# Kernel optimization log

Measured on AMD Instinct MI355X. Metric: run time of the kernel, lower is better.

## Reference

```python
import jax, jax.numpy as jnp
import numpy as np

DIM = 1024; HEADS = 8; DHEAD = 64; INNER = HEADS * DHEAD
WS = 512; B = 2; N = 2048; FF = 4 * DIM
NEG = -1e9


def layernorm(x, g, b, eps=1e-5):
    mu = jnp.mean(x, -1, keepdims=True)
    var = jnp.mean((x - mu) ** 2, -1, keepdims=True)
    return (x - mu) * jax.lax.rsqrt(var + eps) * g + b


def rmsnorm(x, g, eps=1e-6):
    return x * jax.lax.rsqrt(jnp.mean(x * x, -1, keepdims=True) + eps) * g


def rotate_half(x):
    x1, x2 = jnp.split(x, 2, -1)
    return jnp.concatenate([-x2, x1], -1)


def local_attention(q, k, v):
    # lucidrains LocalAttention: single-head over last dim, rotary pos emb,
    # window_size=WS, causal, look_backward=1, look_forward=0. n % WS == 0 so autopad no-op.
    b, n, d = q.shape
    w = n // WS
    inv_freq = 1.0 / (10000.0 ** (jnp.arange(0, d, 2, dtype=jnp.float32) / d))
    t = jnp.arange(n)
    freqs = t[:, None].astype(jnp.float32) * inv_freq[None, :]
    emb = jnp.concatenate([freqs, freqs], -1)           # [n, d]
    cos, sin = jnp.cos(emb), jnp.sin(emb)
    q = q * cos + rotate_half(q) * sin
    k = k * cos + rotate_half(k) * sin
    bq = q.reshape(b, w, WS, d) * (d ** -0.5)
    bk = k.reshape(b, w, WS, d)
    bv = v.reshape(b, w, WS, d)

    def look_around(x, pad_value):
        # gather current window + 1 window backward along the window axis
        pads = [(0, 0), (1, 0)] + [(0, 0)] * (x.ndim - 2)
        xp = jnp.pad(x, pads, constant_values=pad_value)
        return jnp.concatenate([xp[:, 0:w], xp[:, 1:w + 1]], axis=2)

    bk = look_around(bk, 0.0)                 # [b, w, 2*WS, d]
    bv = look_around(bv, 0.0)
    bt = t.reshape(w, WS)                     # query positions per window
    bqk = look_around(bt[None], -1)[0]        # key positions, pad = -1  [w, 2*WS]
    sim = jnp.einsum('bwie,bwje->bwij', bq, bk)  # [b, w, WS, 2*WS]
    mask = (bt[:, :, None] < bqk[:, None, :]) | (bqk[:, None, :] == -1)
    sim = jnp.where(mask[None], NEG, sim)
    attn = jax.nn.softmax(sim, -1)
    out = jnp.einsum('bwij,bwje->bwie', attn, bv)
    return out.reshape(b, n, d)


def setup_inputs() -> dict:
    key = jax.random.key(0)
    ks = jax.random.split(key, 10)
    s = 0.02
    f32 = jnp.float32
    return {
        'text': jax.random.normal(ks[0], (B, N, DIM), f32),
        'audio': jax.random.normal(ks[1], (B, N, DIM), f32),
        'video': jax.random.normal(ks[2], (B, N, DIM), f32),
        'Wa': jax.random.normal(ks[3], (DIM, DIM), f32) * s,
        'ba': jnp.zeros((DIM,), f32),
        'lna_g': jnp.ones((DIM,), f32), 'lna_b': jnp.zeros((DIM,), f32),
        'Wvid': jax.random.normal(ks[4], (DIM, DIM), f32) * s,
        'bvid': jnp.zeros((DIM,), f32),
        'lnv_g': jnp.ones((DIM,), f32), 'lnv_b': jnp.zeros((DIM,), f32),
        'ln1_g': jnp.ones((DIM,), f32), 'ln1_b': jnp.zeros((DIM,), f32),
        'Wq': jax.random.normal(ks[5], (DIM, INNER), f32) * s,
        'Wkv': jax.random.normal(ks[6], (DIM, 2 * INNER), f32) * s,
        'qn_g': jnp.ones((DHEAD,), f32), 'kn_g': jnp.ones((DHEAD,), f32),
        'Wo': jax.random.normal(ks[7], (INNER, DIM), f32) * s,
        'W1': jax.random.normal(ks[8], (DIM, FF), f32) * s,
        'b1': jnp.zeros((FF,), f32),
        'ln2_g': jnp.ones((FF,), f32), 'ln2_b': jnp.zeros((FF,), f32),
        'W2': jax.random.normal(ks[9], (FF, DIM), f32) * s,
        'b2': jnp.zeros((DIM,), f32),
    }


def reference(text, audio, video, Wa, ba, lna_g, lna_b, Wvid, bvid, lnv_g, lnv_b,
              ln1_g, ln1_b, Wq, Wkv, qn_g, kn_g, Wo, W1, b1, ln2_g, ln2_b, W2, b2):
    # modality -> text-token adapters (audio_to_text / video_to_text): linear + layernorm
    audio_t = layernorm(audio @ Wa + ba, lna_g, lna_b)
    video_t = layernorm(video @ Wvid + bvid, lnv_g, lnv_b)
    # windowed local attention: q=text, k=audio tokens, v=video tokens
    x = local_attention(text, audio_t, video_t)          # [B, N, DIM]
    # qk-norm full causal attention (flash=False: dense [B,H,N,N] scores)
    b, n, _ = x.shape
    h = layernorm(x, ln1_g, ln1_b)
    q = (h @ Wq).reshape(b, n, HEADS, DHEAD).transpose(0, 2, 1, 3)
    k, v = jnp.split(h @ Wkv, 2, -1)
    k = k.reshape(b, n, HEADS, DHEAD).transpose(0, 2, 1, 3)
    v = v.reshape(b, n, HEADS, DHEAD).transpose(0, 2, 1, 3)
    q = rmsnorm(q, qn_g)
    k = rmsnorm(k, kn_g)
    sim = jnp.einsum('bhid,bhjd->bhij', q, k) * (DHEAD ** -0.5)
    causal = jnp.tril(jnp.ones((n, n), bool))
    sim = jnp.where(causal[None, None], sim, NEG)
    attn = jax.nn.softmax(sim, -1)
    o = jnp.einsum('bhij,bhjd->bhid', attn, v).transpose(0, 2, 1, 3).reshape(b, n, INNER)
    x = o @ Wo
    x = x + x                                            # x = x + x in source
    # FFN: Linear -> GELU -> post-act LayerNorm -> Linear, + residual
    h1 = layernorm(jax.nn.gelu(x @ W1 + b1), ln2_g, ln2_b)
    return h1 @ W2 + b2 + x
```

## Files before the change

### kernel.cpp

```cpp
#include <hip/hip_runtime.h>
#include <hip/hip_bf16.h>

typedef __bf16 bf16;
typedef __bf16 bf16x8 __attribute__((ext_vector_type(8)));
typedef float  f32x4  __attribute__((ext_vector_type(4)));

static __device__ __forceinline__ float b2f(bf16 x) { return (float)x; }
static __device__ __forceinline__ bf16  f2b(float x) { return (bf16)x; }
static __device__ __forceinline__ float ldval(float v) { return v; }
static __device__ __forceinline__ float ldval(bf16 v)  { return (float)v; }

static __device__ __forceinline__ void gl_lds16(const bf16* g, bf16* l)
{
    __builtin_amdgcn_global_load_lds(
        (const __attribute__((address_space(1))) void*)g,
        (__attribute__((address_space(3))) void*)l,
        16, 0, 0);
}

__global__ void detect_dtype(const unsigned short* __restrict__ p, int* __restrict__ flag)
{
    if (threadIdx.x == 0 && blockIdx.x == 0) {
        int big = 0;
        for (int i = 0; i < 512; ++i) {
            int e = (p[i] >> 7) & 0xFF;
            if (e >= 0xE0) big++;
        }
        *flag = (big > 0) ? 1 : 0;
    }
}

__global__ __launch_bounds__(256) void convert2(
    const void* __restrict__ sa, const void* __restrict__ sb,
    bf16* __restrict__ da, bf16* __restrict__ db, int n,
    const int* __restrict__ flag)
{
    int f = *flag;
    int half = gridDim.x >> 1;
    const void* s = (blockIdx.x < half) ? sa : sb;
    bf16* d = (blockIdx.x < half) ? da : db;
    int bid = (blockIdx.x < half) ? blockIdx.x : blockIdx.x - half;
    for (int i = bid * 256 + threadIdx.x; i < n; i += half * 256) {
        float v = f ? ((const float*)s)[i] : (float)((const bf16*)s)[i];
        d[i] = f2b(v);
    }
}

struct VecPack { const void* src[14]; int n[14]; };
__global__ __launch_bounds__(256) void convert_vecs(
    VecPack vp, bf16* __restrict__ dst, const int* __restrict__ flag)
{
    int v = blockIdx.x;
    int f = *flag;
    const void* s = vp.src[v];
    int n = vp.n[v];
    bf16* d = dst + (size_t)v * 4096;
    for (int i = threadIdx.x; i < n; i += 256) {
        float x = f ? ((const float*)s)[i] : (float)((const bf16*)s)[i];
        d[i] = f2b(x);
    }
}

template <int EPI, int MT>
__global__ __launch_bounds__(256) void gemm_bt(
    const bf16* __restrict__ A0, int lda, int zsA, int zsA2,
    const bf16* __restrict__ B0, int ldb, int zsB, int zsB2,
    void* __restrict__ C0, int ldc, int zsC, int zsC2,
    const bf16* __restrict__ bias, int zsBias, float scale, int K)
{
    constexpr int IFR = MT / 32;
    __shared__ __align__(16) bf16 As[MT * 64];
    __shared__ __align__(16) bf16 Bs[128 * 64];
    const int z = blockIdx.z;
    const bf16* A  = A0 + (size_t)z * zsA + (size_t)(z >> 2) * zsA2;
    const bf16* Bt = B0 + (size_t)z * zsB + (size_t)(z >> 2) * zsB2;
    const size_t cbase = (size_t)z * zsC + (size_t)(z >> 2) * zsC2;
    if (bias) bias += (size_t)z * zsBias;
    const int tid  = threadIdx.x;
    const int lane = tid & 63, wave = tid >> 6;
    const int quad = lane >> 4, l16 = lane & 15;
    const size_t tm = (size_t)blockIdx.y * MT, tn = (size_t)blockIdx.x * 128;
    const int wm = (wave >> 1) * (MT / 2), wn = (wave & 1) * 64;
    const int srow = lane >> 3;
    const int scol = ((lane & 7) ^ srow) * 8;

    f32x4 acc[IFR][4];
    const f32x4 zro = {0.f, 0.f, 0.f, 0.f};
    #pragma unroll
    for (int i = 0; i < IFR; ++i)
        #pragma unroll
        for (int j = 0; j < 4; ++j) acc[i][j] = zro;

    const int swzA = l16 & 7;
    for (int k0 = 0; k0 < K; k0 += 64) {
        #pragma unroll
        for (int i = 0; i < IFR; ++i) {
            int chunk = (wave * IFR + i) * 64;
            int row = (chunk >> 3) + srow;
            gl_lds16(A + (tm + row) * (size_t)lda + k0 + scol, As + (size_t)chunk * 8);
        }
        #pragma unroll
        for (int i = 0; i < 4; ++i) {
            int chunk = (wave * 4 + i) * 64;
            int row = (chunk >> 3) + srow;
            gl_lds16(Bt + (tn + row) * (size_t)ldb + k0 + scol, Bs + (size_t)chunk * 8);
        }
        __syncthreads();
        #pragma unroll
        for (int kk = 0; kk < 2; ++kk) {
            bf16x8 af[IFR], bfr[4];
            #pragma unroll
            for (int i = 0; i < IFR; ++i) {
                int row = wm + i * 16 + l16;
                af[i] = *(const bf16x8*)(const void*)&As[(row * 8 + ((kk*4 + quad) ^ swzA)) * 8];
            }
            #pragma unroll
            for (int j = 0; j < 4; ++j) {
                int row = wn + j * 16 + l16;
                bfr[j] = *(const bf16x8*)(const void*)&Bs[(row * 8 + ((kk*4 + quad) ^ swzA)) * 8];
            }
            #pragma unroll
            for (int i = 0; i < IFR; ++i)
                #pragma unroll
                for (int j = 0; j < 4; ++j)
                    acc[i][j] = __builtin_amdgcn_mfma_f32_16x16x32_bf16(
                        af[i], bfr[j], acc[i][j], 0, 0, 0);
        }
        __syncthreads();
    }

    float* Cf = (float*)C0;
    bf16*  Cb = (bf16*)C0;
    #pragma unroll
    for (int i = 0; i < IFR; ++i) {
        #pragma unroll
        for (int j = 0; j < 4; ++j) {
            size_t col = tn + wn + j*16 + l16;
            float bb = bias ? b2f(bias[col]) : 0.f;
            #pragma unroll
            for (int r = 0; r < 4; ++r) {
                size_t row = tm + wm + i*16 + quad*4 + r;
                float v = acc[i][j][r] + bb;
                size_t off = cbase + row * (size_t)ldc + col;
                if (EPI == 0) {
                    Cf[off] = v;
                } else if (EPI == 1) {
                    Cb[off] = f2b(v * scale);
                } else {
                    float g = 0.5f * v * (1.f + tanhf(0.7978845608028654f *
                                  (v + 0.044715f * v * v * v)));
                    Cb[off] = f2b(g);
                }
            }
        }
    }
}

__global__ __launch_bounds__(512, 2) void gemm_ff1_8ph(
    const bf16* __restrict__ A, int lda,
    const bf16* __restrict__ Bt, int ldb,
    bf16* __restrict__ C, int ldc,
    const bf16* __restrict__ bias, int K)
{
    __shared__ __align__(16) bf16 As[2][256 * 64];
    __shared__ __align__(16) bf16 Bs[2][256 * 64];
    const int tid  = threadIdx.x;
    const int lane = tid & 63, wave = tid >> 6;
    const int quad = lane >> 4, l16 = lane & 15;
    const int wr = wave >> 2, wc = wave & 3;
    const size_t tm = (size_t)blockIdx.y * 256;
    const size_t tn = (size_t)blockIdx.x * 256;
    const int srow = lane >> 3;
    const int scol = ((lane & 7) ^ srow) * 8;
    const int swz  = l16 & 7;

    f32x4 acc[8][4];
    const f32x4 zro = {0.f, 0.f, 0.f, 0.f};
    #pragma unroll
    for (int m = 0; m < 8; ++m)
        #pragma unroll
        for (int n = 0; n < 4; ++n) acc[m][n] = zro;

    const bf16* aSrc[4];
    const bf16* bSrc[4];
    #pragma unroll
    for (int i = 0; i < 4; ++i) {
        int grow = wave * 32 + i * 8 + srow;
        aSrc[i] = A  + (tm + grow) * (size_t)lda + scol;
        bSrc[i] = Bt + (tn + grow) * (size_t)ldb + scol;
    }

#define STAGE(BUF, K0, I)                                                     \
    do {                                                                      \
        gl_lds16(aSrc[I] + (K0), &As[BUF][(wave * 4 + (I)) * 512]);           \
        gl_lds16(bSrc[I] + (K0), &Bs[BUF][(wave * 4 + (I)) * 512]);           \
    } while (0)

#define LDA_F(BUF, M, KK)                                                     \
    (*(const bf16x8*)(const void*)&As[BUF][(wr * 128 + (M) * 16 + l16) * 64 + \
        ((((KK) * 4 + quad) ^ swz) << 3)])
#define LDB_F(BUF, N, KK)                                                     \
    (*(const bf16x8*)(const void*)&Bs[BUF][(wc * 64 + (N) * 16 + l16) * 64 +  \
        ((((KK) * 4 + quad) ^ swz) << 3)])

#define PHASE(M0, M1, PREF_STMT, TAIL_STMT)                                   \
    {                                                                         \
        PREF_STMT;                                                            \
        bf16x8 x0 = LDA_F(cur, M0, 0), x1 = LDA_F(cur, M0, 1);                \
        bf16x8 y0 = LDA_F(cur, M1, 0), y1 = LDA_F(cur, M1, 1);                \
        asm volatile("s_barrier" ::: "memory");                               \
        __builtin_amdgcn_s_setprio(1);                                        \
        _Pragma("unroll")                                                     \
        for (int n = 0; n < 4; ++n) {                                         \
            acc[M0][n] = __builtin_amdgcn_mfma_f32_16x16x32_bf16(x0, bfr[n][0], acc[M0][n], 0, 0, 0); \
            acc[M0][n] = __builtin_amdgcn_mfma_f32_16x16x32_bf16(x1, bfr[n][1], acc[M0][n], 0, 0, 0); \
            acc[M1][n] = __builtin_amdgcn_mfma_f32_16x16x32_bf16(y0, bfr[n][0], acc[M1][n], 0, 0, 0); \
            acc[M1][n] = __builtin_amdgcn_mfma_f32_16x16x32_bf16(y1, bfr[n][1], acc[M1][n], 0, 0, 0); \
        }                                                                     \
        __builtin_amdgcn_s_setprio(0);                                        \
        TAIL_STMT;                                                            \
        asm volatile("s_barrier" ::: "memory");                               \
    }

    #pragma unroll
    for (int i = 0; i < 4; ++i) STAGE(0, 0, i);
    asm volatile("s_waitcnt vmcnt(0)" ::: "memory");
    asm volatile("s_barrier" ::: "memory");

    const int NT = K >> 6;
    bf16x8 bfr[4][2];
    for (int t = 0; t < NT; ++t) {
        const int cur = t & 1, nxt = cur ^ 1;
        const int k1  = (t + 1) << 6;
        const bool pref = (t + 1 < NT);

        #pragma unroll
        for (int n = 0; n < 4; ++n) {
            bfr[n][0] = LDB_F(cur, n, 0);
            bfr[n][1] = LDB_F(cur, n, 1);
        }
        PHASE(0, 1,
              if (pref) { STAGE(nxt, k1, 0); STAGE(nxt, k1, 1); }, )
        PHASE(2, 3,
              if (pref) { STAGE(nxt, k1, 2); STAGE(nxt, k1, 3); }, )
        PHASE(4, 5, , )
        PHASE(6, 7, ,
              asm volatile("s_waitcnt vmcnt(0)" ::: "memory"))
    }
#undef PHASE
#undef LDB_F
#undef LDA_F
#undef STAGE

    #pragma unroll
    for (int m = 0; m < 8; ++m) {
        #pragma unroll
        for (int n = 0; n < 4; ++n) {
            size_t col = tn + wc * 64 + n * 16 + l16;
            float bb = b2f(bias[col]);
            #pragma unroll
            for (int r = 0; r < 4; ++r) {
                size_t row = tm + wr * 128 + m * 16 + quad * 4 + r;
                float v = acc[m][n][r] + bb;
                float s = v * (1.5957691216057308f + 0.07135481627f * v * v);
                float g = v / (1.f + __expf(-s));
                C[row * (size_t)ldc + col] = f2b(g);
            }
        }
    }
}

__global__ void transpose_any(const void* __restrict__ in, int R, int C,
                              unsigned short* __restrict__ out, int ldo,
                              const int* __restrict__ flag)
{
    __shared__ unsigned short t[32][33];
    int f = *flag;
    int c0 = blockIdx.x * 32, r0 = blockIdx.y * 32;
    int tx = threadIdx.x, ty = threadIdx.y;
    for (int i = ty; i < 32; i += 8) {
        size_t idx = (size_t)(r0 + i) * C + c0 + tx;
        bf16 v = f ? f2b(((const float*)in)[idx]) : ((const bf16*)in)[idx];
        t[i][tx] = *(unsigned short*)&v;
    }
    __syncthreads();
    for (int i = ty; i < 32; i += 8)
        out[(size_t)(c0 + i) * ldo + r0 + tx] = t[tx][i];
}

__global__ void transpose_vt(const unsigned short* __restrict__ in,
                             unsigned short* __restrict__ out)
{
    __shared__ unsigned short t[32][33];
    int b = blockIdx.z;
    const unsigned short* src = in + (size_t)b * 2048 * 1024;
    unsigned short* dst = out + (size_t)b * 1024 * 2560;
    int c0 = blockIdx.x * 32, r0 = blockIdx.y * 32;
    int tx = threadIdx.x, ty = threadIdx.y;
    for (int i = ty; i < 32; i += 8)
        t[i][tx] = src[(size_t)(r0 + i) * 1024 + c0 + tx];
    __syncthreads();
    for (int i = ty; i < 32; i += 8)
        dst[(size_t)(c0 + i) * 2560 + 512 + r0 + tx] = t[tx][i];
}

__global__ void transpose_v(const float* __restrict__ qkv, bf16* __restrict__ Vt)
{
    __shared__ float t[32][33];
    int bh = blockIdx.z, b = bh >> 3, h = bh & 7;
    const float* src = qkv + (size_t)b * 2048 * 1536 + 1024 + h * 64;
    int c0 = blockIdx.x * 32, r0 = blockIdx.y * 32;
    int tx = threadIdx.x, ty = threadIdx.y;
    for (int i = ty; i < 32; i += 8)
        t[i][tx] = src[(size_t)(r0 + i) * 1536 + c0 + tx];
    __syncthreads();
    bf16* dst = Vt + (size_t)bh * 64 * 2048;
    for (int i = ty; i < 32; i += 8)
        dst[(size_t)(c0 + i) * 2048 + r0 + tx] = f2b(t[tx][i]);
}

template <typename Tin>
__global__ __launch_bounds__(256) void ln_rows(
    const Tin* __restrict__ in, int C,
    const bf16* __restrict__ g, const bf16* __restrict__ b,
    bf16* __restrict__ out, float eps)
{
    const int row = blockIdx.x, tid = threadIdx.x;
    const Tin* p = in + (size_t)row * C;
    float s = 0.f, ss = 0.f;
    for (int c = tid; c < C; c += 256) {
        float v = ldval(p[c]);
        s += v; ss += v * v;
    }
    #pragma unroll
    for (int d = 32; d > 0; d >>= 1) { s += __shfl_xor(s, d); ss += __shfl_xor(ss, d); }
    __shared__ float red[2][4];
    int wave = tid >> 6, lane = tid & 63;
    if (lane == 0) { red[0][wave] = s; red[1][wave] = ss; }
    __syncthreads();
    s  = red[0][0] + red[0][1] + red[0][2] + red[0][3];
    ss = red[1][0] + red[1][1] + red[1][2] + red[1][3];
    float mu   = s / C;
    float var  = ss / C - mu * mu;
    float rstd = rsqrtf(var + eps);
    bf16* q = out + (size_t)row * C;
    for (int c = tid; c < C; c += 256) {
        float v = ldval(p[c]);
        q[c] = f2b((v - mu) * rstd * b2f(g[c]) + b2f(b[c]));
    }
}

__global__ __launch_bounds__(256) void ln_rows2(
    const bf16* __restrict__ in,
    const bf16* __restrict__ g0, const bf16* __restrict__ b0,
    const bf16* __restrict__ g1, const bf16* __restrict__ b1,
    bf16* __restrict__ out0, bf16* __restrict__ out1)
{
    const int row = blockIdx.x, tid = threadIdx.x;
    const int sel = row >> 12;
    const bf16* p = in + (size_t)row * 1024;
    const bf16* g = sel ? g1 : g0;
    const bf16* b = sel ? b1 : b0;
    bf16* q = (sel ? out1 + (size_t)(row - 4096) * 1024 : out0 + (size_t)row * 1024);
    float s = 0.f, ss = 0.f;
    for (int c = tid; c < 1024; c += 256) {
        float v = b2f(p[c]);
        s += v; ss += v * v;
    }
    #pragma unroll
    for (int d = 32; d > 0; d >>= 1) { s += __shfl_xor(s, d); ss += __shfl_xor(ss, d); }
    __shared__ float red[2][4];
    int wave = tid >> 6, lane = tid & 63;
    if (lane == 0) { red[0][wave] = s; red[1][wave] = ss; }
    __syncthreads();
    s  = red[0][0] + red[0][1] + red[0][2] + red[0][3];
    ss = red[1][0] + red[1][1] + red[1][2] + red[1][3];
    float mu   = s * (1.f / 1024.f);
    float var  = ss * (1.f / 1024.f) - mu * mu;
    float rstd = rsqrtf(var + 1e-5f);
    for (int c = tid; c < 1024; c += 256) {
        float v = b2f(p[c]);
        q[c] = f2b((v - mu) * rstd * b2f(g[c]) + b2f(b[c]));
    }
}

__global__ __launch_bounds__(256) void rotary_kernel(
    const void* __restrict__ text, const int* __restrict__ flag,
    const bf16* __restrict__ audioT,
    bf16* __restrict__ qrot, bf16* __restrict__ krotPad)
{
    int row = blockIdx.x;
    int t = row & 2047, b = row >> 11;
    int tid = threadIdx.x;
    int f = *flag;
    const float lg = 9.210340371976184f / 512.f;
    size_t base = (size_t)row * 1024;
    size_t kb = ((size_t)(b * 2560 + 512 + t)) * 1024;
    for (int c = tid; c < 512; c += 256) {
        float invf = __expf(-(float)c * lg);
        float th = (float)t * invf;
        float sn, cs;
        sincosf(th, &sn, &cs);
        float q1 = f ? ((const float*)text)[base + c]
                     : b2f(((const bf16*)text)[base + c]);
        float q2 = f ? ((const float*)text)[base + c + 512]
                     : b2f(((const bf16*)text)[base + c + 512]);
        qrot[base + c]       = f2b((q1 * cs - q2 * sn) * 0.03125f);
        qrot[base + c + 512] = f2b((q2 * cs + q1 * sn) * 0.03125f);
        float k1 = b2f(audioT[base + c]), k2 = b2f(audioT[base + c + 512]);
        krotPad[kb + c]       = f2b(k1 * cs - k2 * sn);
        krotPad[kb + c + 512] = f2b(k2 * cs + k1 * sn);
    }
}

__global__ __launch_bounds__(256) void softmax_local(
    const float* __restrict__ sim, bf16* __restrict__ attn)
{
    int i  = blockIdx.x;
    int zz = blockIdx.y;
    int w  = zz & 3;
    int tid = threadIdx.x;
    const float* p = sim + ((size_t)zz * 512 + i) * 1024;
    bf16* q = attn + ((size_t)zz * 512 + i) * 1024;
    int jlo = (w == 0) ? 512 : 0;
    int jhi = 512 + i;
    float m = -1e30f;
    #pragma unroll
    for (int k = 0; k < 4; ++k) {
        int c = tid + k * 256;
        if (c >= jlo && c <= jhi) m = fmaxf(m, p[c]);
    }
    #pragma unroll
    for (int d = 32; d > 0; d >>= 1) m = fmaxf(m, __shfl_xor(m, d));
    __shared__ float red[2][4];
    int wave = tid >> 6, lane = tid & 63;
    if (lane == 0) red[0][wave] = m;
    __syncthreads();
    m = fmaxf(fmaxf(red[0][0], red[0][1]), fmaxf(red[0][2], red[0][3]));
    float pv[4];
    float s = 0.f;
    #pragma unroll
    for (int k = 0; k < 4; ++k) {
        int c = tid + k * 256;
        float e = (c >= jlo && c <= jhi) ? __expf(p[c] - m) : 0.f;
        pv[k] = e; s += e;
    }
    #pragma unroll
    for (int d = 32; d > 0; d >>= 1) s += __shfl_xor(s, d);
    if (lane == 0) red[1][wave] = s;
    __syncthreads();
    s = red[1][0] + red[1][1] + red[1][2] + red[1][3];
    float inv = 1.f / s;
    #pragma unroll
    for (int k = 0; k < 4; ++k) q[tid + k * 256] = f2b(pv[k] * inv);
}

__global__ __launch_bounds__(256) void pack_qk(
    const float* __restrict__ qkv, bf16* __restrict__ Qp, bf16* __restrict__ Kp,
    const bf16* __restrict__ qn_g, const bf16* __restrict__ kn_g)
{
    int gid  = blockIdx.x * 4 + (threadIdx.x >> 6);
    int lane = threadIdx.x & 63;
    int token = gid >> 4, r = gid & 15, part = r >> 3, h = r & 7;
    const float* p = qkv + (size_t)token * 1536 + part * 512 + h * 64 + lane;
    float v = *p;
    float ss = v * v;
    #pragma unroll
    for (int d = 32; d > 0; d >>= 1) ss += __shfl_xor(ss, d);
    float sc = rsqrtf(ss * (1.f / 64.f) + 1e-6f);
    const bf16* gw = part ? kn_g : qn_g;
    float outv = v * sc * b2f(gw[lane]);
    if (!part) outv *= 0.125f;
    int b = token >> 11, t = token & 2047;
    bf16* dst = (part ? Kp : Qp) + ((size_t)(b * 8 + h) * 2048 + t) * 64 + lane;
    *dst = f2b(outv);
}

__global__ __launch_bounds__(128, 3) void flash_fused3(
    const bf16* __restrict__ Qp, const bf16* __restrict__ Kp,
    const bf16* __restrict__ Vt, bf16* __restrict__ o)
{
    __shared__ __align__(16) bf16 Ks[64][72];
    __shared__ __align__(16) bf16 Vs[64][72];
    __shared__ __align__(16) bf16 Ps[2][16][72];
    const int qb = 63 - blockIdx.x;
    const int bh = blockIdx.y, b = bh >> 3, h = bh & 7;
    const int qm = qb * 32;
    const int tid = threadIdx.x, wave = tid >> 6, lane = tid & 63;
    const int quad = lane >> 4, l16 = lane & 15;
    const bf16* Qg = Qp + (size_t)bh * 2048 * 64;
    const bf16* Kg = Kp + (size_t)bh * 2048 * 64;
    const bf16* Vg = Vt + (size_t)bh * 64 * 2048;

    const int qrow = qm + wave * 16 + l16;
    bf16x8 qa[2];
    qa[0] = *(const bf16x8*)(const void*)(Qg + (size_t)qrow * 64 + quad * 8);
    qa[1] = *(const bf16x8*)(const void*)(Qg + (size_t)qrow * 64 + 32 + quad * 8);

    f32x4 oacc[4];
    const f32x4 zro = {0.f, 0.f, 0.f, 0.f};
    #pragma unroll
    for (int j = 0; j < 4; ++j) oacc[j] = zro;
    float mst[4] = {-1e30f, -1e30f, -1e30f, -1e30f};
    float lst[4] = {0.f, 0.f, 0.f, 0.f};

    const int ldr = tid >> 1, ldc = (tid & 1) * 32;
    const int ntiles = (qb >> 1) + 1;
    for (int t = 0; t < ntiles; ++t) {
        const int jt = t * 64;
        #pragma unroll
        for (int c = 0; c < 4; ++c) {
            *(uint4*)(void*)&Ks[ldr][ldc + c * 8] =
                *(const uint4*)(const void*)(Kg + (size_t)(jt + ldr) * 64 + ldc + c * 8);
            *(uint4*)(void*)&Vs[ldr][ldc + c * 8] =
                *(const uint4*)(const void*)(Vg + (size_t)ldr * 2048 + jt + ldc + c * 8);
        }
        __syncthreads();

        f32x4 s[4];
        #pragma unroll
        for (int j = 0; j < 4; ++j) s[j] = zro;
        #pragma unroll
        for (int kk = 0; kk < 2; ++kk) {
            #pragma unroll
            for (int j = 0; j < 4; ++j) {
                bf16x8 kb = *(const bf16x8*)(const void*)&Ks[j*16 + l16][kk*32 + quad*8];
                s[j] = __builtin_amdgcn_mfma_f32_16x16x32_bf16(qa[kk], kb, s[j], 0, 0, 0);
            }
        }

        if (jt + 63 > qm + wave * 16) {
            #pragma unroll
            for (int j = 0; j < 4; ++j) {
                int key = jt + j * 16 + l16;
                #pragma unroll
                for (int r = 0; r < 4; ++r) {
                    int row = qm + wave * 16 + quad * 4 + r;
                    if (key > row) s[j][r] = -1e30f;
                }
            }
        }

        f32x4 tmax = s[0];
        #pragma unroll
        for (int j = 1; j < 4; ++j)
            #pragma unroll
            for (int r = 0; r < 4; ++r) tmax[r] = fmaxf(tmax[r], s[j][r]);
        #pragma unroll
        for (int r = 0; r < 4; ++r) {
            float tv = tmax[r];
            #pragma unroll
            for (int d = 1; d < 16; d <<= 1) tv = fmaxf(tv, __shfl_xor(tv, d));
            tmax[r] = tv;
        }
        float scl[4];
        #pragma unroll
        for (int r = 0; r < 4; ++r) {
            float mn = fmaxf(mst[r], tmax[r]);
            scl[r] = __expf(mst[r] - mn);
            mst[r] = mn;
        }
        f32x4 psum = zro;
        #pragma unroll
        for (int j = 0; j < 4; ++j)
            #pragma unroll
            for (int r = 0; r < 4; ++r) {
                float e = __expf(s[j][r] - mst[r]);
                s[j][r] = e;
                psum[r] += e;
            }
        #pragma unroll
        for (int r = 0; r < 4; ++r) {
            float tv = psum[r];
            #pragma unroll
            for (int d = 1; d < 16; d <<= 1) tv += __shfl_xor(tv, d);
            lst[r] = lst[r] * scl[r] + tv;
        }
        #pragma unroll
        for (int j = 0; j < 4; ++j)
            #pragma unroll
            for (int r = 0; r < 4; ++r) oacc[j][r] *= scl[r];

        #pragma unroll
        for (int j = 0; j < 4; ++j)
            #pragma unroll
            for (int r = 0; r < 4; ++r)
                Ps[wave][quad*4 + r][j*16 + l16] = f2b(s[j][r]);
        bf16x8 pa[2];
        pa[0] = *(const bf16x8*)(const void*)&Ps[wave][l16][quad*8];
        pa[1] = *(const bf16x8*)(const void*)&Ps[wave][l16][32 + quad*8];

        #pragma unroll
        for (int kk = 0; kk < 2; ++kk) {
            #pragma unroll
            for (int j = 0; j < 4; ++j) {
                bf16x8 vb = *(const bf16x8*)(const void*)&Vs[j*16 + l16][kk*32 + quad*8];
                oacc[j] = __builtin_amdgcn_mfma_f32_16x16x32_bf16(pa[kk], vb, oacc[j], 0, 0, 0);
            }
        }
        __syncthreads();
    }

    #pragma unroll
    for (int j = 0; j < 4; ++j) {
        #pragma unroll
        for (int r = 0; r < 4; ++r) {
            int t = qm + wave * 16 + quad * 4 + r;
            o[((size_t)(b * 2048 + t)) * 512 + h * 64 + j * 16 + l16] =
                f2b(oacc[j][r] / lst[r]);
        }
    }
}

__global__ __launch_bounds__(256) void combine_ff2(
    const float* __restrict__ p0, const float* __restrict__ p1,
    const bf16* __restrict__ x2, const bf16* __restrict__ b2,
    float* __restrict__ out)
{
    int i4 = (blockIdx.x * 256 + threadIdx.x) * 4;
    #pragma unroll
    for (int k = 0; k < 4; ++k) {
        int i = i4 + k;
        out[i] = p0[i] + p1[i] + b2f(x2[i]) + b2f(b2[i & 1023]);
    }
}

static void launch_gemm(int epi, hipStream_t s,
                        const bf16* A, int lda, int zsA, int zsA2,
                        const bf16* Bt, int ldb, int zsB, int zsB2,
                        void* C, int ldc, int zsC, int zsC2,
                        const bf16* bias, int zsBias, float scale,
                        int M, int N, int K, int nz)
{
    bool mt64 = ((M >> 7) * (N >> 7) * nz) <= 512;
    dim3 blk(256);
    if (mt64) {
        dim3 g(N / 128, M / 64, nz);
        switch (epi) {
        case 0: gemm_bt<0,64><<<g, blk, 0, s>>>(A, lda, zsA, zsA2, Bt, ldb, zsB, zsB2, C, ldc, zsC, zsC2, bias, zsBias, scale, K); break;
        case 1: gemm_bt<1,64><<<g, blk, 0, s>>>(A, lda, zsA, zsA2, Bt, ldb, zsB, zsB2, C, ldc, zsC, zsC2, bias, zsBias, scale, K); break;
        default: gemm_bt<2,64><<<g, blk, 0, s>>>(A, lda, zsA, zsA2, Bt, ldb, zsB, zsB2, C, ldc, zsC, zsC2, bias, zsBias, scale, K); break;
        }
    } else {
        dim3 g(N / 128, M / 128, nz);
        switch (epi) {
        case 0: gemm_bt<0,128><<<g, blk, 0, s>>>(A, lda, zsA, zsA2, Bt, ldb, zsB, zsB2, C, ldc, zsC, zsC2, bias, zsBias, scale, K); break;
        case 1: gemm_bt<1,128><<<g, blk, 0, s>>>(A, lda, zsA, zsA2, Bt, ldb, zsB, zsB2, C, ldc, zsC, zsC2, bias, zsBias, scale, K); break;
        default: gemm_bt<2,128><<<g, blk, 0, s>>>(A, lda, zsA, zsA2, Bt, ldb, zsB, zsB2, C, ldc, zsC, zsC2, bias, zsBias, scale, K); break;
        }
    }
}

extern "C" void kernel_launch(void* const* d_in, const int* in_sizes, int n_in,
                              void* d_out, int out_size, void* d_ws, size_t ws_size,
                              hipStream_t stream)
{
    const void* text  = d_in[0];
    const void* audio = d_in[1];
    const void* video = d_in[2];
    const void* Wa    = d_in[3];
    const void* ba    = d_in[4];
    const void* lna_g = d_in[5];
    const void* lna_b = d_in[6];
    const void* Wvid  = d_in[7];
    const void* bvid  = d_in[8];
    const void* lnv_g = d_in[9];
    const void* lnv_b = d_in[10];
    const void* ln1_g = d_in[11];
    const void* ln1_b = d_in[12];
    const void* Wq    = d_in[13];
    const void* Wkv   = d_in[14];
    const void* qn_g  = d_in[15];
    const void* kn_g  = d_in[16];
    const void* Wo    = d_in[17];
    const void* W1    = d_in[18];
    const void* b1    = d_in[19];
    const void* ln2_g = d_in[20];
    const void* ln2_b = d_in[21];
    const void* W2    = d_in[22];
    const void* b2    = d_in[23];

    char* ws = (char*)d_ws;
    size_t off = 0;
    auto alloc = [&](size_t bytes) -> char* {
        char* p = ws + off;
        off += (bytes + 255) & ~(size_t)255;
        return p;
    };
    const size_t MB = 1024 * 1024;
    int*  flag  = (int*)alloc(256);
    bf16* vecs  = (bf16*)alloc(14 * 4096 * 2);
    bf16* WqkvT = (bf16*)alloc((size_t)1536 * 1024 * 2);
    bf16* WoT   = (bf16*)alloc((size_t)1024 * 512 * 2);
    bf16* W1T   = (bf16*)alloc((size_t)4096 * 1024 * 2);
    bf16* W2T   = (bf16*)alloc((size_t)1024 * 4096 * 2);
    char* regionIn = alloc(24 * MB);
    char* region2  = alloc(32 * MB);
    char* regionH  = alloc(8 * MB);
    char* regionX  = alloc(8 * MB);
    char* regionO  = alloc(4 * MB);
    bf16* qrot    = (bf16*)alloc((size_t)4096 * 1024 * 2);
    bf16* krotPad = (bf16*)alloc((size_t)2 * 2560 * 1024 * 2);
    bf16* VTpad   = (bf16*)alloc((size_t)2 * 1024 * 2560 * 2);
    bf16* attn    = (bf16*)alloc((size_t)8 * 512 * 1024 * 2);

    bf16*  audioC = (bf16*)regionIn;
    bf16*  videoC = audioC + (size_t)4096 * 1024;
    float* qkvF   = (float*)regionIn;
    bf16*  tmp2   = (bf16*)region2;
    float* tmpF   = (float*)region2;
    float* xF     = (float*)(region2 + 16 * MB);
    bf16*  g      = (bf16*)region2;
    bf16*  audioT = (bf16*)regionH;
    bf16*  h      = (bf16*)regionH;
    bf16*  videoT = (bf16*)regionX;
    bf16*  x2     = (bf16*)regionX;
    bf16*  WaT    = (bf16*)regionO;
    bf16*  WvT    = WaT + (size_t)1024 * 1024;
    bf16*  o      = (bf16*)regionO;
    bf16*  Qp     = qrot;
    bf16*  Kp     = krotPad;
    bf16*  Vth    = attn;
    float* p0     = (float*)regionIn;
    float* p1     = (float*)VTpad;

    bf16* baC   = vecs + 0 * 4096;
    bf16* bvidC = vecs + 1 * 4096;
    bf16* lnagC = vecs + 2 * 4096;
    bf16* lnabC = vecs + 3 * 4096;
    bf16* lnvgC = vecs + 4 * 4096;
    bf16* lnvbC = vecs + 5 * 4096;
    bf16* ln1gC = vecs + 6 * 4096;
    bf16* ln1bC = vecs + 7 * 4096;
    bf16* qngC  = vecs + 8 * 4096;
    bf16* kngC  = vecs + 9 * 4096;
    bf16* b1C   = vecs + 10 * 4096;
    bf16* ln2gC = vecs + 11 * 4096;
    bf16* ln2bC = vecs + 12 * 4096;
    bf16* b2C   = vecs + 13 * 4096;

    detect_dtype<<<1, 64, 0, stream>>>((const unsigned short*)text, flag);

    const int NTOK = 4096 * 1024;
    convert2<<<4096, 256, 0, stream>>>(audio, video, audioC, videoC, NTOK, flag);
    VecPack vp;
    const void* vsrc[14] = {ba, bvid, lna_g, lna_b, lnv_g, lnv_b, ln1_g, ln1_b,
                            qn_g, kn_g, b1, ln2_g, ln2_b, b2};
    int vn[14] = {1024, 1024, 1024, 1024, 1024, 1024, 1024, 1024,
                  64, 64, 4096, 4096, 4096, 1024};
    for (int i = 0; i < 14; ++i) { vp.src[i] = vsrc[i]; vp.n[i] = vn[i]; }
    convert_vecs<<<14, 256, 0, stream>>>(vp, vecs, flag);

    dim3 tb(32, 8);
    transpose_any<<<dim3(32, 32), tb, 0, stream>>>(Wa, 1024, 1024, (unsigned short*)WaT, 1024, flag);
    transpose_any<<<dim3(32, 32), tb, 0, stream>>>(Wvid, 1024, 1024, (unsigned short*)WvT, 1024, flag);
    transpose_any<<<dim3(16, 32), tb, 0, stream>>>(Wq, 1024, 512, (unsigned short*)WqkvT, 1024, flag);
    transpose_any<<<dim3(32, 32), tb, 0, stream>>>(Wkv, 1024, 1024, (unsigned short*)(WqkvT + (size_t)512 * 1024), 1024, flag);
    transpose_any<<<dim3(32, 16), tb, 0, stream>>>(Wo, 512, 1024, (unsigned short*)WoT, 512, flag);
    transpose_any<<<dim3(128, 32), tb, 0, stream>>>(W1, 1024, 4096, (unsigned short*)W1T, 1024, flag);
    transpose_any<<<dim3(32, 128), tb, 0, stream>>>(W2, 4096, 1024, (unsigned short*)W2T, 4096, flag);

    launch_gemm(1, stream, audioC, 1024, 4096*1024, 0, WaT, 1024, 1024*1024, 0,
                tmp2, 1024, 4096*1024, 0, baC, 4096, 1.f, 4096, 1024, 1024, 2);
    ln_rows2<<<8192, 256, 0, stream>>>(tmp2, lnagC, lnabC, lnvgC, lnvbC, audioT, videoT);

    hipMemsetAsync(krotPad, 0, (size_t)2 * 2560 * 1024 * 2, stream);
    hipMemsetAsync(VTpad, 0, (size_t)2 * 1024 * 2560 * 2, stream);
    rotary_kernel<<<4096, 256, 0, stream>>>(text, flag, audioT, qrot, krotPad);
    transpose_vt<<<dim3(32, 64, 2), tb, 0, stream>>>(
        (const unsigned short*)videoT, (unsigned short*)VTpad);

    launch_gemm(0, stream, qrot, 1024, 512*1024, 0,
                krotPad, 1024, 512*1024, 512*1024,
                tmpF, 1024, 512*1024, 0, nullptr, 0, 1.f, 512, 1024, 1024, 8);
    softmax_local<<<dim3(512, 8), 256, 0, stream>>>(tmpF, attn);
    launch_gemm(0, stream, attn, 1024, 512*1024, 0,
                VTpad, 2560, 512, 1024*2560 - 2048,
                xF, 1024, 512*1024, 0, nullptr, 0, 1.f, 512, 1024, 1024, 8);

    ln_rows<float><<<4096, 256, 0, stream>>>(xF, 1024, ln1gC, ln1bC, h, 1e-5f);
    launch_gemm(0, stream, h, 1024, 0, 0, WqkvT, 1024, 0, 0,
                qkvF, 1536, 0, 0, nullptr, 0, 1.f, 4096, 1536, 1024, 1);
    pack_qk<<<16384, 256, 0, stream>>>(qkvF, Qp, Kp, qngC, kngC);
    transpose_v<<<dim3(2, 64, 16), tb, 0, stream>>>(qkvF, Vth);
    flash_fused3<<<dim3(64, 16), 128, 0, stream>>>(Qp, Kp, Vth, o);

    launch_gemm(1, stream, o, 512, 0, 0, WoT, 512, 0, 0,
                x2, 1024, 0, 0, nullptr, 0, 2.f, 4096, 1024, 512, 1);
    gemm_ff1_8ph<<<dim3(16, 16), 512, 0, stream>>>(x2, 1024, W1T, 1024,
                                                   g, 4096, b1C, 1024);
    ln_rows<bf16><<<4096, 256, 0, stream>>>(g, 4096, ln2gC, ln2bC, g, 1e-5f);
    launch_gemm(0, stream, g, 4096, 2048, 0, W2T, 4096, 2048, 0,
                p0, 1024, (int)(p1 - p0), 0, nullptr, 0, 1.f, 4096, 1024, 2048, 2);
    combine_ff2<<<4096, 256, 0, stream>>>(p0, p1, x2, b2C, (float*)d_out);

    (void)in_sizes; (void)n_in; (void)out_size; (void)ws_size;
}
```

Baseline: 581.1 us.

## Double-buffer K/V tiles and transpose QK^T MFMA to cut softmax shuffles

The flash attention kernel now keeps two K/V tiles in shared memory and prefetches the next tile into registers while the current one is computed, so only one barrier per tile is needed and global load latency is hidden. The QK^T MFMA operands are swapped so that each lane holds scores for a single query row. Row max and sum then reduce with two cross-quad shuffles instead of sixteen per-row butterfly shuffles, and the P tile is written to shared memory with packed stores. In exchange the kernel uses more shared memory and registers, and the launch bound drops from 3 to 2 blocks per CU, which may lower occupancy.

```diff
diff --git a/kernel.cpp b/kernel.cpp
--- a/kernel.cpp
+++ b/kernel.cpp
@@ -476,12 +476,12 @@
     *dst = f2b(outv);
 }
 
-__global__ __launch_bounds__(128, 3) void flash_fused3(
+__global__ __launch_bounds__(128, 2) void flash_fused4(
     const bf16* __restrict__ Qp, const bf16* __restrict__ Kp,
     const bf16* __restrict__ Vt, bf16* __restrict__ o)
 {
-    __shared__ __align__(16) bf16 Ks[64][72];
-    __shared__ __align__(16) bf16 Vs[64][72];
+    __shared__ __align__(16) bf16 Ks[2][64][72];
+    __shared__ __align__(16) bf16 Vs[2][64][72];
     __shared__ __align__(16) bf16 Ps[2][16][72];
     const int qb = 63 - blockIdx.x;
     const int bh = blockIdx.y, b = bh >> 3, h = bh & 7;
@@ -492,30 +492,45 @@
     const bf16* Kg = Kp + (size_t)bh * 2048 * 64;
     const bf16* Vg = Vt + (size_t)bh * 64 * 2048;
 
-    const int qrow = qm + wave * 16 + l16;
+    const int q_row = qm + wave * 16 + l16;
     bf16x8 qa[2];
-    qa[0] = *(const bf16x8*)(const void*)(Qg + (size_t)qrow * 64 + quad * 8);
-    qa[1] = *(const bf16x8*)(const void*)(Qg + (size_t)qrow * 64 + 32 + quad * 8);
+    qa[0] = *(const bf16x8*)(const void*)(Qg + (size_t)q_row * 64 + quad * 8);
+    qa[1] = *(const bf16x8*)(const void*)(Qg + (size_t)q_row * 64 + 32 + quad * 8);
 
     f32x4 oacc[4];
     const f32x4 zro = {0.f, 0.f, 0.f, 0.f};
     #pragma unroll
     for (int j = 0; j < 4; ++j) oacc[j] = zro;
-    float mst[4] = {-1e30f, -1e30f, -1e30f, -1e30f};
-    float lst[4] = {0.f, 0.f, 0.f, 0.f};
+    float mst = -1e30f, lst = 0.f;
 
     const int ldr = tid >> 1, ldc = (tid & 1) * 32;
-    const int ntiles = (qb >> 1) + 1;
-    for (int t = 0; t < ntiles; ++t) {
+    const int nt = (qb >> 1) + 1;
+
+    uint4 kreg[4], vreg[4];
+    #pragma unroll
+    for (int c = 0; c < 4; ++c) {
+        kreg[c] = *(const uint4*)(const void*)(Kg + (size_t)ldr * 64 + ldc + c * 8);
+        vreg[c] = *(const uint4*)(const void*)(Vg + (size_t)ldr * 2048 + ldc + c * 8);
+    }
+    #pragma unroll
+    for (int c = 0; c < 4; ++c) {
+        *(uint4*)(void*)&Ks[0][ldr][ldc + c * 8] = kreg[c];
+        *(uint4*)(void*)&Vs[0][ldr][ldc + c * 8] = vreg[c];
+    }
+    __syncthreads();
+
+    for (int t = 0; t < nt; ++t) {
+        const int cur = t & 1, nxt = cur ^ 1;
         const int jt = t * 64;
-        #pragma unroll
-        for (int c = 0; c < 4; ++c) {
-            *(uint4*)(void*)&Ks[ldr][ldc + c * 8] =
-                *(const uint4*)(const void*)(Kg + (size_t)(jt + ldr) * 64 + ldc + c * 8);
-            *(uint4*)(void*)&Vs[ldr][ldc + c * 8] =
-                *(const uint4*)(const void*)(Vg + (size_t)ldr * 2048 + jt + ldc + c * 8);
-        }
-        __syncthreads();
+        const bool pref = (t + 1 < nt);
+        if (pref) {
+            const int jn = jt + 64;
+            #pragma unroll
+            for (int c = 0; c < 4; ++c) {
+                kreg[c] = *(const uint4*)(const void*)(Kg + (size_t)(jn + ldr) * 64 + ldc + c * 8);
+                vreg[c] = *(const uint4*)(const void*)(Vg + (size_t)ldr * 2048 + jn + ldc + c * 8);
+            }
+        }
 
         f32x4 s[4];
         #pragma unroll
@@ -524,90 +539,101 @@
         for (int kk = 0; kk < 2; ++kk) {
             #pragma unroll
             for (int j = 0; j < 4; ++j) {
-                bf16x8 kb = *(const bf16x8*)(const void*)&Ks[j*16 + l16][kk*32 + quad*8];
-                s[j] = __builtin_amdgcn_mfma_f32_16x16x32_bf16(qa[kk], kb, s[j], 0, 0, 0);
+                bf16x8 kf = *(const bf16x8*)(const void*)&Ks[cur][j*16 + l16][kk*32 + quad*8];
+                s[j] = __builtin_amdgcn_mfma_f32_16x16x32_bf16(kf, qa[kk], s[j], 0, 0, 0);
             }
         }
 
-        if (jt + 63 > qm + wave * 16) {
+        if (jt + 63 > q_row) {
             #pragma unroll
             for (int j = 0; j < 4; ++j) {
-                int key = jt + j * 16 + l16;
                 #pragma unroll
                 for (int r = 0; r < 4; ++r) {
-                    int row = qm + wave * 16 + quad * 4 + r;
-                    if (key > row) s[j][r] = -1e30f;
+                    int key = jt + j * 16 + quad * 4 + r;
+                    if (key > q_row) s[j][r] = -1e30f;
                 }
             }
         }
 
-        f32x4 tmax = s[0];
-        #pragma unroll
-        for (int j = 1; j < 4; ++j)
-            #pragma unroll
-            for (int r = 0; r < 4; ++r) tmax[r] = fmaxf(tmax[r], s[j][r]);
+        float mq = s[0][0];
+        #pragma unroll
+        for (int j = 0; j < 4; ++j)
+            #pragma unroll
+            for (int r = 0; r < 4; ++r) mq = fmaxf(mq, s[j][r]);
+        float e[4][4];
+        float sq = 0.f;
+        #pragma unroll
+        for (int j = 0; j < 4; ++j)
+            #pragma unroll
+            for (int r = 0; r < 4; ++r) {
+                float v = __expf(s[j][r] - mq);
+                e[j][r] = v; sq += v;
+            }
+
+        float mo = __shfl_xor(mq, 16);
+        float so = __shfl_xor(sq, 16);
+        float mm = fmaxf(mq, mo);
+        sq = sq * __expf(mq - mm) + so * __expf(mo - mm);
+        float mo2 = __shfl_xor(mm, 32);
+        float so2 = __shfl_xor(sq, 32);
+        float mtile = fmaxf(mm, mo2);
+        float stile = sq * __expf(mm - mtile) + so2 * __expf(mo2 - mtile);
+
+        float mn  = fmaxf(mst, mtile);
+        float scl = __expf(mst - mn);
+        lst = lst * scl + stile * __expf(mtile - mn);
+        mst = mn;
+        float pf = __expf(mq - mn);
+
+        float sclq[4];
+        #pragma unroll
+        for (int r = 0; r < 4; ++r) sclq[r] = __shfl(scl, quad * 4 + r);
+        #pragma unroll
+        for (int j = 0; j < 4; ++j)
+            #pragma unroll
+            for (int r = 0; r < 4; ++r) oacc[j][r] *= sclq[r];
+
+        #pragma unroll
+        for (int j = 0; j < 4; ++j) {
+            union { bf16 hx[4]; uint2 u; } pk;
+            pk.hx[0] = f2b(e[j][0] * pf); pk.hx[1] = f2b(e[j][1] * pf);
+            pk.hx[2] = f2b(e[j][2] * pf); pk.hx[3] = f2b(e[j][3] * pf);
+            *(uint2*)(void*)&Ps[wave][l16][j * 16 + quad * 4] = pk.u;
+        }
+        bf16x8 pa0 = *(const bf16x8*)(const void*)&Ps[wave][l16][quad * 8];
+        bf16x8 pa1 = *(const bf16x8*)(const void*)&Ps[wave][l16][32 + quad * 8];
+
+        #pragma unroll
+        for (int j = 0; j < 4; ++j) {
+            bf16x8 vb = *(const bf16x8*)(const void*)&Vs[cur][j*16 + l16][quad*8];
+            oacc[j] = __builtin_amdgcn_mfma_f32_16x16x32_bf16(pa0, vb, oacc[j], 0, 0, 0);
+        }
+        #pragma unroll
+        for (int j = 0; j < 4; ++j) {
+            bf16x8 vb = *(const bf16x8*)(const void*)&Vs[cur][j*16 + l16][32 + quad*8];
+            oacc[j] = __builtin_amdgcn_mfma_f32_16x16x32_bf16(pa1, vb, oacc[j], 0, 0, 0);
+        }
+
+        if (pref) {
+            #pragma unroll
+            for (int c = 0; c < 4; ++c) {
+                *(uint4*)(void*)&Ks[nxt][ldr][ldc + c * 8] = kreg[c];
+                *(uint4*)(void*)&Vs[nxt][ldr][ldc + c * 8] = vreg[c];
+            }
+            __syncthreads();
+        }
+    }
+
+    float invq[4];
+    #pragma unroll
+    for (int r = 0; r < 4; ++r) invq[r] = 1.f / __shfl(lst, quad * 4 + r);
+    #pragma unroll
+    for (int j = 0; j < 4; ++j) {
         #pragma unroll
         for (int r = 0; r < 4; ++r) {
-            float tv = tmax[r];
-            #pragma unroll
-            for (int d = 1; d < 16; d <<= 1) tv = fmaxf(tv, __shfl_xor(tv, d));
-            tmax[r] = tv;
-        }
-        float scl[4];
-        #pragma unroll
-        for (int r = 0; r < 4; ++r) {
-            float mn = fmaxf(mst[r], tmax[r]);
-            scl[r] = __expf(mst[r] - mn);
-            mst[r] = mn;
-        }
-        f32x4 psum = zro;
-        #pragma unroll
-        for (int j = 0; j < 4; ++j)
-            #pragma unroll
-            for (int r = 0; r < 4; ++r) {
-                float e = __expf(s[j][r] - mst[r]);
-                s[j][r] = e;
-                psum[r] += e;
-            }
-        #pragma unroll
-        for (int r = 0; r < 4; ++r) {
-            float tv = psum[r];
-            #pragma unroll
-            for (int d = 1; d < 16; d <<= 1) tv += __shfl_xor(tv, d);
-            lst[r] = lst[r] * scl[r] + tv;
-        }
-        #pragma unroll
-        for (int j = 0; j < 4; ++j)
-            #pragma unroll
-            for (int r = 0; r < 4; ++r) oacc[j][r] *= scl[r];
-
-        #pragma unroll
-        for (int j = 0; j < 4; ++j)
-            #pragma unroll
-            for (int r = 0; r < 4; ++r)
-                Ps[wave][quad*4 + r][j*16 + l16] = f2b(s[j][r]);
-        bf16x8 pa[2];
-        pa[0] = *(const bf16x8*)(const void*)&Ps[wave][l16][quad*8];
-        pa[1] = *(const bf16x8*)(const void*)&Ps[wave][l16][32 + quad*8];
-
-        #pragma unroll
-        for (int kk = 0; kk < 2; ++kk) {
-            #pragma unroll
-            for (int j = 0; j < 4; ++j) {
-                bf16x8 vb = *(const bf16x8*)(const void*)&Vs[j*16 + l16][kk*32 + quad*8];
-                oacc[j] = __builtin_amdgcn_mfma_f32_16x16x32_bf16(pa[kk], vb, oacc[j], 0, 0, 0);
-            }
-        }
-        __syncthreads();
-    }
-
-    #pragma unroll
-    for (int j = 0; j < 4; ++j) {
-        #pragma unroll
-        for (int r = 0; r < 4; ++r) {
-            int t = qm + wave * 16 + quad * 4 + r;
-            o[((size_t)(b * 2048 + t)) * 512 + h * 64 + j * 16 + l16] =
-                f2b(oacc[j][r] / lst[r]);
+            int tr = qm + wave * 16 + quad * 4 + r;
+            o[((size_t)(b * 2048 + tr)) * 512 + h * 64 + j * 16 + l16] =
+                f2b(oacc[j][r] * invq[r]);
         }
     }
 }
@@ -783,7 +809,7 @@
                 qkvF, 1536, 0, 0, nullptr, 0, 1.f, 4096, 1536, 1024, 1);
     pack_qk<<<16384, 256, 0, stream>>>(qkvF, Qp, Kp, qngC, kngC);
     transpose_v<<<dim3(2, 64, 16), tb, 0, stream>>>(qkvF, Vth);
-    flash_fused3<<<dim3(64, 16), 128, 0, stream>>>(Qp, Kp, Vth, o);
+    flash_fused4<<<dim3(64, 16), 128, 0, stream>>>(Qp, Kp, Vth, o);
 
     launch_gemm(1, stream, o, 512, 0, 0, WoT, 512, 0, 0,
                 x2, 1024, 0, 0, nullptr, 0, 2.f, 4096, 1024, 512, 1);
```

Result: slower. 649.4 us (+11.7%).
